# Performance work log

Hardware: AMD Instinct MI355X
Metric: run time of the kernel (lower is better)

## Reference

```python
import jax, jax.numpy as jnp
import numpy as np

N = 50000      # nodes
E = 800000     # edges
F = 128        # num_features
H = 128        # hidden_channels
L = 3          # num_layers
P = 32         # num_partitions
EPS = 1e-5     # BatchNorm1d eps


def _batchnorm(h):
    # BatchNorm1d(affine=False, track_running_stats=False): batch stats, biased var
    m = jnp.mean(h, axis=0)
    v = jnp.var(h, axis=0)
    return (h - m) * jax.lax.rsqrt(v + EPS)


def setup_inputs() -> dict:
    key = jax.random.key(0)
    ks = jax.random.split(key, 12)
    x = jax.random.normal(ks[0], (N, F), dtype=jnp.float32)
    edge_index = jax.random.randint(ks[1], (2, E), 0, N)
    edge_weights = jax.random.uniform(ks[2], (E,), dtype=jnp.float32)
    partitions = (jax.random.uniform(ks[3], (N, P)) < (1.0 / P)).astype(jnp.float32)
    node_weights = jax.random.uniform(ks[4], (N,), dtype=jnp.float32)
    edge_curr_node = jax.random.uniform(ks[5], (N,), dtype=jnp.float32)
    conv_w = 0.05 * jax.random.normal(ks[6], (L, F, H), dtype=jnp.float32)
    conv_b = jnp.zeros((L, H), dtype=jnp.float32)
    lin1_w = 0.05 * jax.random.normal(ks[7], (4 * H, H), dtype=jnp.float32)
    lin1_b = jnp.zeros((H,), dtype=jnp.float32)
    lin2_w = 0.05 * jax.random.normal(ks[8], (H, 1), dtype=jnp.float32)
    lin2_b = jnp.zeros((1,), dtype=jnp.float32)
    return {"x": x, "edge_index": edge_index, "edge_weights": edge_weights,
            "partitions": partitions, "node_weights": node_weights,
            "edge_curr_node": edge_curr_node, "conv_w": conv_w, "conv_b": conv_b,
            "lin1_w": lin1_w, "lin1_b": lin1_b, "lin2_w": lin2_w,
            "lin2_b": lin2_b, "curr_node_id": 123}


def reference(x, edge_index, edge_weights, partitions, node_weights,
              edge_curr_node, conv_w, conv_b, lin1_w, lin1_b, lin2_w, lin2_b,
              curr_node_id):
    src, dst = edge_index[0], edge_index[1]
    # GCN normalization with added self-loops (weight 1)
    deg = jax.ops.segment_sum(edge_weights, dst, num_segments=N) + 1.0
    dinv = jax.lax.rsqrt(deg)
    norm = dinv[src] * edge_weights * dinv[dst]          # [E]
    self_norm = (dinv * dinv)[:, None]                   # [N,1]

    h = x
    for l in range(L):
        hw = h @ conv_w[l] + conv_b[l]                   # [N,H]
        agg = jax.ops.segment_sum(hw[src] * norm[:, None], dst, num_segments=N)
        agg = agg + hw * self_norm                       # self-loop term
        h = jax.nn.relu(_batchnorm(agg))

    x_curr = h[curr_node_id]                             # [H]
    # mlp scoring: concat [h | x_curr | edge_col repeated to 2H] -> [N,4H]
    cat = jnp.concatenate([
        h,
        jnp.broadcast_to(x_curr[None, :], (N, H)),
        jnp.broadcast_to(edge_curr_node[:, None], (N, 2 * H)),
    ], axis=1)
    scores = jax.nn.relu(cat @ lin1_w + lin1_b) @ lin2_w + lin2_b  # [N,1]
    # pool == 'sum'
    partition_scores = scores.T @ partitions             # [1,P]
    return (partition_scores, h)
```

## Files before the change

### kernel.cpp

```cpp
#include <hip/hip_runtime.h>

#define N_NODES 50000
#define N_EDGES 800000
#define NP 50048
#define MAXDEG 64
#define PADK 136
#define NCOPY 64
#define WPB 512
#define NBUK 196
#define BCAP 6144
#define EBB 782

typedef __bf16 bf16_8 __attribute__((ext_vector_type(8)));
typedef float  f32_4  __attribute__((ext_vector_type(4)));

__device__ inline float2 bf2f2(unsigned int u) {
    union { unsigned int i; float f; } a, b;
    a.i = u << 16;
    b.i = u & 0xffff0000u;
    return make_float2(a.f, b.f);
}

__global__ void k_init_wprep(float* __restrict__ colpart, float* __restrict__ out_head,
                             const float* __restrict__ conv_w, const float* __restrict__ lin1_w,
                             __bf16* __restrict__ WT, float* __restrict__ svec,
                             int* __restrict__ bcnt) {
    int b = blockIdx.x, t = threadIdx.x;
    if (b < WPB) {
        int mat = b >> 7, n = b & 127;
        if (t < 128) {
            const float* srcm = (mat < 3) ? (conv_w + (size_t)mat * 16384) : lin1_w;
            WT[((size_t)mat * 128 + n) * 128 + t] = (__bf16)srcm[(size_t)t * 128 + n];
        }
    } else if (b == WPB) {
        if (t < 128) {
            float s = 0.f;
            for (int k = 256; k < 512; ++k) s += lin1_w[(size_t)k * 128 + t];
            svec[t] = s;
        }
    } else if (b < WPB + 65) {
        int i = (b - WPB - 1) * 256 + t;
        colpart[i] = 0.f;
    } else {
        if (t < 32) out_head[t] = 0.f;
        for (int i = t; i < NBUK * 16; i += 256) bcnt[i] = 0;
    }
}

__global__ __launch_bounds__(1024) void k_bucket(const int* __restrict__ src,
                                                 const int* __restrict__ dst,
                                                 const float* __restrict__ ew,
                                                 int* __restrict__ bcnt,
                                                 uint2* __restrict__ ebuf) {
    __shared__ uint2 stage[1024];
    __shared__ int cnt[NBUK], cnt2[NBUK], lstart[NBUK], gb[NBUK];
    __shared__ int wtot[4];
    int t = threadIdx.x;
    int e0 = blockIdx.x * 1024;
    int tot = min(1024, N_EDGES - e0);
    if (t < NBUK) { cnt[t] = 0; cnt2[t] = 0; }
    __syncthreads();
    uint2 rec = make_uint2(0u, 0u); int b = -1;
    if (t < tot) {
        int e = e0 + t;
        unsigned s = (unsigned)src[e], d = (unsigned)dst[e];
        rec = make_uint2(s | (d << 16), __float_as_uint(ew[e]));
        b = (int)(d >> 8);
        atomicAdd(&cnt[b], 1);
    }
    __syncthreads();
    int c = (t < NBUK) ? cnt[t] : 0;
    int x = c;
#pragma unroll
    for (int d2 = 1; d2 < 64; d2 <<= 1) {
        int v = __shfl_up(x, d2, 64);
        if ((t & 63) >= d2) x += v;
    }
    if ((t & 63) == 63 && t < 256) wtot[t >> 6] = x;
    if (t < NBUK && c > 0) gb[t] = atomicAdd(&bcnt[t * 16], c);
    __syncthreads();
    if (t < NBUK) {
        int pre = x - c;
        for (int w = 0; w < (t >> 6); ++w) pre += wtot[w];
        lstart[t] = pre;
    }
    __syncthreads();
    if (t < tot) {
        int r = atomicAdd(&cnt2[b], 1);
        stage[lstart[b] + r] = rec;
    }
    __syncthreads();
    if (t < tot) {
        uint2 v = stage[t];
        int bb = (int)(v.x >> 24);
        int idx = gb[bb] + (t - lstart[bb]);
        if (idx < BCAP) ebuf[(size_t)bb * BCAP + idx] = v;
    }
}

__global__ __launch_bounds__(256) void k_build(const int* __restrict__ bcnt,
                                               const uint2* __restrict__ ebuf,
                                               uint2* __restrict__ esn,
                                               int* __restrict__ fillp,
                                               float* __restrict__ dinv) {
    __shared__ int cnt[256];
    __shared__ float wsum[256];
    int t = threadIdx.x, b = blockIdx.x;
    cnt[t] = 0; wsum[t] = 0.f;
    __syncthreads();
    int m = min(bcnt[b * 16], BCAP);
    for (int i = t; i < m; i += 256) {
        uint2 rec = ebuf[(size_t)b * BCAP + i];
        int d = (int)(rec.x >> 16);
        int local = d & 255;
        int pos = atomicAdd(&cnt[local], 1);
        if (pos < MAXDEG)
            esn[(size_t)d * MAXDEG + pos] = make_uint2(rec.x & 0xffffu, rec.y);
        atomicAdd(&wsum[local], __uint_as_float(rec.y));
    }
    __syncthreads();
    int gn = b * 256 + t;
    if (gn < N_NODES) {
        fillp[gn] = cnt[t];
        dinv[gn] = rsqrtf(1.0f + wsum[t]);
    }
}

template <int AMODE>
__global__ __launch_bounds__(256) void k_gemm_mfma(const float* __restrict__ A,
                                                   const float* __restrict__ mean,
                                                   const float* __restrict__ rstd,
                                                   const __bf16* __restrict__ WT,
                                                   const float* __restrict__ bias,
                                                   __bf16* __restrict__ C, int nrows,
                                                   uint2* __restrict__ esn,
                                                   const int* __restrict__ fillp,
                                                   const float* __restrict__ dinv,
                                                   int gemmBlocks) {
    __shared__ __bf16 As[64 * PADK];
    __shared__ __bf16 Ws[128 * PADK];
    int t = threadIdx.x;
    if (AMODE == 0 && blockIdx.x >= gemmBlocks) {
        int n = ((blockIdx.x - gemmBlocks) * 256 + t) >> 6;
        int lane = t & 63;
        if (n >= N_NODES) return;
        int num = min(fillp[n], MAXDEG);
        if (lane < num) {
            uint2 e = esn[(size_t)n * MAXDEG + lane];
            float w = dinv[(int)e.x] * __uint_as_float(e.y) * dinv[n];
            esn[(size_t)n * MAXDEG + lane] = make_uint2(e.x, __float_as_uint(w));
        }
        return;
    }
    int rowBase = blockIdx.x * 64;
    const uint4* WTg = (const uint4*)WT;
    for (int i = t; i < 2048; i += 256) {
        int n = i >> 4, k8 = i & 15;
        *(uint4*)&Ws[n * PADK + k8 * 8] = WTg[i];
    }
    const float4* A4 = (const float4*)A;
    const float4* M4 = (const float4*)mean;
    const float4* R4 = (const float4*)rstd;
    for (int i = t; i < 1024; i += 256) {
        int r = i >> 4, k8 = i & 15;
        int gr = rowBase + r;
        float4 a0 = make_float4(0.f, 0.f, 0.f, 0.f), a1 = a0;
        if (gr < nrows) {
            a0 = A4[(size_t)gr * 32 + k8 * 2];
            a1 = A4[(size_t)gr * 32 + k8 * 2 + 1];
        }
        if (AMODE == 1) {
            float4 m0 = M4[k8 * 2], m1 = M4[k8 * 2 + 1];
            float4 r0 = R4[k8 * 2], r1 = R4[k8 * 2 + 1];
            a0.x = fmaxf((a0.x - m0.x) * r0.x, 0.f); a0.y = fmaxf((a0.y - m0.y) * r0.y, 0.f);
            a0.z = fmaxf((a0.z - m0.z) * r0.z, 0.f); a0.w = fmaxf((a0.w - m0.w) * r0.w, 0.f);
            a1.x = fmaxf((a1.x - m1.x) * r1.x, 0.f); a1.y = fmaxf((a1.y - m1.y) * r1.y, 0.f);
            a1.z = fmaxf((a1.z - m1.z) * r1.z, 0.f); a1.w = fmaxf((a1.w - m1.w) * r1.w, 0.f);
        }
        bf16_8 o = { (__bf16)a0.x, (__bf16)a0.y, (__bf16)a0.z, (__bf16)a0.w,
                     (__bf16)a1.x, (__bf16)a1.y, (__bf16)a1.z, (__bf16)a1.w };
        *(bf16_8*)&As[r * PADK + k8 * 8] = o;
    }
    __syncthreads();
    int wave = t >> 6, lane = t & 63, quad = lane >> 4, m = lane & 15;
    int ar = wave * 16 + m;
    f32_4 acc[8];
#pragma unroll
    for (int i = 0; i < 8; ++i) acc[i] = (f32_4){0.f, 0.f, 0.f, 0.f};
#pragma unroll
    for (int kk = 0; kk < 4; ++kk) {
        bf16_8 a = *(const bf16_8*)&As[ar * PADK + kk * 32 + quad * 8];
#pragma unroll
        for (int n0 = 0; n0 < 8; ++n0) {
            bf16_8 b = *(const bf16_8*)&Ws[(n0 * 16 + m) * PADK + kk * 32 + quad * 8];
            acc[n0] = __builtin_amdgcn_mfma_f32_16x16x32_bf16(a, b, acc[n0], 0, 0, 0);
        }
    }
    __syncthreads();
#pragma unroll
    for (int n0 = 0; n0 < 8; ++n0) {
        int col = n0 * 16 + m;
        float bi = bias[col];
#pragma unroll
        for (int r = 0; r < 4; ++r) {
            int rr = wave * 16 + quad * 4 + r;
            As[rr * PADK + col] = (__bf16)(acc[n0][r] + bi);
        }
    }
    __syncthreads();
    uint4* Cg = (uint4*)C;
    for (int i = t; i < 1024; i += 256) {
        int r = i >> 4, k8 = i & 15;
        int gr = rowBase + r;
        if (gr < nrows) Cg[(size_t)gr * 16 + k8] = *(const uint4*)&As[r * PADK + k8 * 8];
    }
}

__global__ __launch_bounds__(256) void k_agg(const __bf16* __restrict__ hwb,
                                             const uint2* __restrict__ esn,
                                             const int* __restrict__ fillp,
                                             const float* __restrict__ dinv,
                                             float* __restrict__ agg,
                                             float* __restrict__ colpart) {
    __shared__ float red1[4 * 128], red2[4 * 128];
    int t = threadIdx.x;
    int n = (blockIdx.x * 256 + t) >> 6;
    int lane = t & 63, wave = t >> 6;
    int rs = lane >> 4, c16 = lane & 15;
    float acc[8];
#pragma unroll
    for (int k = 0; k < 8; ++k) acc[k] = 0.f;
    const uint4* hwq = (const uint4*)hwb;
    if (n < N_NODES) {
        int num = min(fillp[n], MAXDEG);
        float dvn = dinv[n];
        uint4 sv = hwq[(size_t)n * 16 + c16];
        int s_l = 0; float w_l = 0.f;
        if (lane < num) {
            uint2 e = esn[(size_t)n * MAXDEG + lane];
            s_l = (int)e.x;
            w_l = __uint_as_float(e.y);
        }
        int groups = (num + 3) >> 2;
        int g = 0;
        for (; g + 4 <= groups; g += 4) {
            uint4 u[4]; float w[4];
#pragma unroll
            for (int j = 0; j < 4; ++j) {
                int idx = (g + j) * 4 + rs;
                int s = __shfl(s_l, idx, 64);
                w[j] = __shfl(w_l, idx, 64);
                u[j] = hwq[(size_t)s * 16 + c16];
            }
#pragma unroll
            for (int j = 0; j < 4; ++j) {
                float2 f0 = bf2f2(u[j].x), f1 = bf2f2(u[j].y);
                float2 f2 = bf2f2(u[j].z), f3 = bf2f2(u[j].w);
                acc[0] += f0.x * w[j]; acc[1] += f0.y * w[j];
                acc[2] += f1.x * w[j]; acc[3] += f1.y * w[j];
                acc[4] += f2.x * w[j]; acc[5] += f2.y * w[j];
                acc[6] += f3.x * w[j]; acc[7] += f3.y * w[j];
            }
        }
        for (; g < groups; ++g) {
            int idx = g * 4 + rs;
            int s = __shfl(s_l, idx, 64);
            float w = __shfl(w_l, idx, 64);
            uint4 u = hwq[(size_t)s * 16 + c16];
            float2 f0 = bf2f2(u.x), f1 = bf2f2(u.y), f2 = bf2f2(u.z), f3 = bf2f2(u.w);
            acc[0] += f0.x * w; acc[1] += f0.y * w;
            acc[2] += f1.x * w; acc[3] += f1.y * w;
            acc[4] += f2.x * w; acc[5] += f2.y * w;
            acc[6] += f3.x * w; acc[7] += f3.y * w;
        }
#pragma unroll
        for (int k = 0; k < 8; ++k) {
            acc[k] += __shfl_xor(acc[k], 16, 64);
            acc[k] += __shfl_xor(acc[k], 32, 64);
        }
        float d2 = dvn * dvn;
        float2 s0 = bf2f2(sv.x), s1 = bf2f2(sv.y), s2 = bf2f2(sv.z), s3 = bf2f2(sv.w);
        acc[0] += s0.x * d2; acc[1] += s0.y * d2;
        acc[2] += s1.x * d2; acc[3] += s1.y * d2;
        acc[4] += s2.x * d2; acc[5] += s2.y * d2;
        acc[6] += s3.x * d2; acc[7] += s3.y * d2;
        if (rs < 2) {
            float4 o = make_float4(acc[rs * 4 + 0], acc[rs * 4 + 1],
                                   acc[rs * 4 + 2], acc[rs * 4 + 3]);
            ((float4*)agg)[(size_t)n * 32 + c16 * 2 + rs] = o;
        }
    }
    if (rs == 0) {
        *(float4*)&red1[wave * 128 + c16 * 8 + 0] =
            make_float4(acc[0], acc[1], acc[2], acc[3]);
        *(float4*)&red1[wave * 128 + c16 * 8 + 4] =
            make_float4(acc[4], acc[5], acc[6], acc[7]);
        *(float4*)&red2[wave * 128 + c16 * 8 + 0] =
            make_float4(acc[0] * acc[0], acc[1] * acc[1], acc[2] * acc[2], acc[3] * acc[3]);
        *(float4*)&red2[wave * 128 + c16 * 8 + 4] =
            make_float4(acc[4] * acc[4], acc[5] * acc[5], acc[6] * acc[6], acc[7] * acc[7]);
    }
    __syncthreads();
    if (t < 128) {
        float s = red1[t] + red1[128 + t] + red1[256 + t] + red1[384 + t];
        float q = red2[t] + red2[128 + t] + red2[256 + t] + red2[384 + t];
        int c = blockIdx.x & (NCOPY - 1);
        unsafeAtomicAdd(&colpart[c * 128 + t], s);
        unsafeAtomicAdd(&colpart[NCOPY * 128 + c * 128 + t], q);
    }
}

__global__ void k_bnfinal(float* colpart, float* mean, float* rstd) {
    int j = threadIdx.x;
    float s = 0.f, q = 0.f;
    for (int c = 0; c < NCOPY; ++c) {
        s += colpart[c * 128 + j];
        q += colpart[NCOPY * 128 + c * 128 + j];
        colpart[c * 128 + j] = 0.f;
        colpart[NCOPY * 128 + c * 128 + j] = 0.f;
    }
    float m = s * (1.0f / N_NODES);
    float v = q * (1.0f / N_NODES) - m * m;
    mean[j] = m;
    rstd[j] = rsqrtf(v + 1e-5f);
}

__global__ void k_prep(const float* __restrict__ agg, const float* __restrict__ mean,
                       const float* __restrict__ rstd, const int* __restrict__ cid,
                       const float* __restrict__ lin1w, const float* __restrict__ lin1b,
                       float* c0) {
    __shared__ float xc[128];
    int t = threadIdx.x;
    int cn = cid[0];
    float a = agg[(size_t)cn * 128 + t];
    xc[t] = fmaxf((a - mean[t]) * rstd[t], 0.f);
    __syncthreads();
    float acc = lin1b[t];
    for (int k = 0; k < 128; ++k)
        acc += xc[k] * lin1w[(size_t)(128 + k) * 128 + t];
    c0[t] = acc;
}

__global__ __launch_bounds__(256) void k_score_mfma(const float* __restrict__ agg,
                                                    const float* __restrict__ mean,
                                                    const float* __restrict__ rstd,
                                                    const __bf16* __restrict__ WT,
                                                    const float* __restrict__ c0,
                                                    const float* __restrict__ svec,
                                                    const float* __restrict__ ecn,
                                                    const float* __restrict__ lin2w,
                                                    const float* __restrict__ lin2b,
                                                    float* __restrict__ scores,
                                                    float* __restrict__ hout,
                                                    int nrows) {
    __shared__ __bf16 As[64 * PADK];
    __shared__ __bf16 Ws[128 * PADK];
    __shared__ float c0s[128], svs[128], l2s[128];
    int t = threadIdx.x;
    int rowBase = blockIdx.x * 64;
    const uint4* WTg = (const uint4*)WT;
    for (int i = t; i < 2048; i += 256) {
        int n = i >> 4, k8 = i & 15;
        *(uint4*)&Ws[n * PADK + k8 * 8] = WTg[i];
    }
    const float4* A4 = (const float4*)agg;
    const float4* M4 = (const float4*)mean;
    const float4* R4 = (const float4*)rstd;
    float4* H4 = (float4*)hout;
    for (int i = t; i < 1024; i += 256) {
        int r = i >> 4, k8 = i & 15;
        int gr = rowBase + r;
        float4 a0 = make_float4(0.f, 0.f, 0.f, 0.f), a1 = a0;
        if (gr < nrows) {
            a0 = A4[(size_t)gr * 32 + k8 * 2];
            a1 = A4[(size_t)gr * 32 + k8 * 2 + 1];
        }
        float4 m0 = M4[k8 * 2], m1 = M4[k8 * 2 + 1];
        float4 r0 = R4[k8 * 2], r1 = R4[k8 * 2 + 1];
        float4 f0, f1;
        f0.x = fmaxf((a0.x - m0.x) * r0.x, 0.f); f0.y = fmaxf((a0.y - m0.y) * r0.y, 0.f);
        f0.z = fmaxf((a0.z - m0.z) * r0.z, 0.f); f0.w = fmaxf((a0.w - m0.w) * r0.w, 0.f);
        f1.x = fmaxf((a1.x - m1.x) * r1.x, 0.f); f1.y = fmaxf((a1.y - m1.y) * r1.y, 0.f);
        f1.z = fmaxf((a1.z - m1.z) * r1.z, 0.f); f1.w = fmaxf((a1.w - m1.w) * r1.w, 0.f);
        if (gr < nrows) {
            H4[(size_t)gr * 32 + k8 * 2] = f0;
            H4[(size_t)gr * 32 + k8 * 2 + 1] = f1;
        }
        bf16_8 o = { (__bf16)f0.x, (__bf16)f0.y, (__bf16)f0.z, (__bf16)f0.w,
                     (__bf16)f1.x, (__bf16)f1.y, (__bf16)f1.z, (__bf16)f1.w };
        *(bf16_8*)&As[r * PADK + k8 * 8] = o;
    }
    if (t < 128) { c0s[t] = c0[t]; svs[t] = svec[t]; l2s[t] = lin2w[t]; }
    __syncthreads();
    int wave = t >> 6, lane = t & 63, quad = lane >> 4, m = lane & 15;
    int ar = wave * 16 + m;
    f32_4 acc[8];
#pragma unroll
    for (int i = 0; i < 8; ++i) acc[i] = (f32_4){0.f, 0.f, 0.f, 0.f};
#pragma unroll
    for (int kk = 0; kk < 4; ++kk) {
        bf16_8 a = *(const bf16_8*)&As[ar * PADK + kk * 32 + quad * 8];
#pragma unroll
        for (int n0 = 0; n0 < 8; ++n0) {
            bf16_8 b = *(const bf16_8*)&Ws[(n0 * 16 + m) * PADK + kk * 32 + quad * 8];
            acc[n0] = __builtin_amdgcn_mfma_f32_16x16x32_bf16(a, b, acc[n0], 0, 0, 0);
        }
    }
    float l2b = lin2b[0];
#pragma unroll
    for (int r = 0; r < 4; ++r) {
        int row = rowBase + wave * 16 + quad * 4 + r;
        float e = (row < nrows) ? ecn[row] : 0.f;
        float partial = 0.f;
#pragma unroll
        for (int n0 = 0; n0 < 8; ++n0) {
            int col = n0 * 16 + m;
            float v = acc[n0][r] + c0s[col] + e * svs[col];
            partial += fmaxf(v, 0.f) * l2s[col];
        }
        partial += __shfl_xor(partial, 8, 16);
        partial += __shfl_xor(partial, 4, 16);
        partial += __shfl_xor(partial, 2, 16);
        partial += __shfl_xor(partial, 1, 16);
        if (m == 0 && row < nrows) scores[row] = partial + l2b;
    }
}

__global__ void k_partition(const float* __restrict__ scores, const float* __restrict__ part,
                            float* out) {
    __shared__ float red[256];
    int t = threadIdx.x;
    int p = t & 31, rg = t >> 5;
    float acc = 0.f;
    for (int r = blockIdx.x * 8 + rg; r < N_NODES; r += gridDim.x * 8)
        acc += scores[r] * part[(size_t)r * 32 + p];
    red[t] = acc;
    __syncthreads();
    if (t < 32) {
        float s = 0.f;
        for (int i = 0; i < 8; ++i) s += red[i * 32 + t];
        unsafeAtomicAdd(&out[t], s);
    }
}

extern "C" void kernel_launch(void* const* d_in, const int* in_sizes, int n_in,
                              void* d_out, int out_size, void* d_ws, size_t ws_size,
                              hipStream_t stream) {
    const float* x        = (const float*)d_in[0];
    const int*   eidx     = (const int*)d_in[1];
    const float* ew       = (const float*)d_in[2];
    const float* parts    = (const float*)d_in[3];
    const float* ecn      = (const float*)d_in[5];
    const float* conv_w   = (const float*)d_in[6];
    const float* conv_b   = (const float*)d_in[7];
    const float* lin1_w   = (const float*)d_in[8];
    const float* lin1_b   = (const float*)d_in[9];
    const float* lin2_w   = (const float*)d_in[10];
    const float* lin2_b   = (const float*)d_in[11];
    const int*   cid      = (const int*)d_in[12];

    const int* src = eidx;
    const int* dst = eidx + N_EDGES;

    char* p = (char*)d_ws;
    auto alloc = [&](size_t bytes) { char* r = p; p += (bytes + 255) & ~size_t(255); return r; };
    int*    fillp   = (int*)alloc((size_t)NP * 4);
    uint2*  esn     = (uint2*)alloc((size_t)N_NODES * MAXDEG * 8);
    float*  dinv    = (float*)alloc(NP * 4);
    float*  scores  = (float*)alloc(NP * 4);
    float*  colpart = (float*)alloc(2 * NCOPY * 128 * 4);
    float*  mean    = (float*)alloc(128 * 4);
    float*  rstd    = (float*)alloc(128 * 4);
    float*  c0      = (float*)alloc(128 * 4);
    float*  svec    = (float*)alloc(128 * 4);
    __bf16* WT      = (__bf16*)alloc(4 * 128 * 128 * 2);
    __bf16* hwb     = (__bf16*)alloc((size_t)N_NODES * 128 * 2);
    float*  agg     = (float*)alloc((size_t)N_NODES * 128 * 4);
    int*    bcnt    = (int*)alloc((size_t)NBUK * 16 * 4);
    uint2*  ebuf    = (uint2*)alloc((size_t)NBUK * BCAP * 8);

    float* out_head = (float*)d_out;
    float* hbuf     = (float*)d_out + 32;

    const int GB = (N_NODES + 63) / 64;
    const int AB = (N_NODES * 64 + 255) / 256;

    k_init_wprep<<<WPB + 66, 256, 0, stream>>>(colpart, out_head, conv_w, lin1_w, WT, svec, bcnt);
    k_bucket<<<EBB, 1024, 0, stream>>>(src, dst, ew, bcnt, ebuf);
    k_build<<<NBUK, 256, 0, stream>>>(bcnt, ebuf, esn, fillp, dinv);

    for (int l = 0; l < 3; ++l) {
        if (l == 0)
            k_gemm_mfma<0><<<GB + AB, 256, 0, stream>>>(x, mean, rstd, WT, conv_b, hwb, N_NODES,
                                                        esn, fillp, dinv, GB);
        else
            k_gemm_mfma<1><<<GB, 256, 0, stream>>>(agg, mean, rstd, WT + (size_t)l * 16384,
                                                   conv_b + (size_t)l * 128, hwb, N_NODES,
                                                   nullptr, nullptr, nullptr, GB);
        k_agg<<<AB, 256, 0, stream>>>(hwb, esn, fillp, dinv, agg, colpart);
        k_bnfinal<<<1, 128, 0, stream>>>(colpart, mean, rstd);
    }

    k_prep<<<1, 128, 0, stream>>>(agg, mean, rstd, cid, lin1_w, lin1_b, c0);
    k_score_mfma<<<GB, 256, 0, stream>>>(agg, mean, rstd, WT + (size_t)3 * 16384, c0, svec,
                                         ecn, lin2_w, lin2_b, scores, hbuf, N_NODES);
    k_partition<<<256, 256, 0, stream>>>(scores, parts, out_head);
}
```

Before: 344.3 us.

## Replace padded per-node edge slots with compact CSR-style packed edge list

The per-node adjacency storage moves from a fixed 64-slot padded array to a compact packed array. Row offsets come from a block-local prefix scan over in-degree counts, and k_build makes a second pass over the bucket to scatter edges. Consumers now read edges at rowofs[n]+lane, which shrinks the footprint and should give denser cache lines for edge-list reads. In exchange k_build reads the bucket twice, adds a scan, and performs an extra rowofs load per node.

```diff
diff --git a/kernel.cpp b/kernel.cpp
--- a/kernel.cpp
+++ b/kernel.cpp
@@ -100,28 +100,49 @@
 
 __global__ __launch_bounds__(256) void k_build(const int* __restrict__ bcnt,
                                                const uint2* __restrict__ ebuf,
-                                               uint2* __restrict__ esn,
+                                               uint2* __restrict__ packed,
+                                               int* __restrict__ rowofs,
                                                int* __restrict__ fillp,
                                                float* __restrict__ dinv) {
     __shared__ int cnt[256];
     __shared__ float wsum[256];
+    __shared__ int pos[256];
+    __shared__ int wtot[4];
     int t = threadIdx.x, b = blockIdx.x;
     cnt[t] = 0; wsum[t] = 0.f;
     __syncthreads();
     int m = min(bcnt[b * 16], BCAP);
     for (int i = t; i < m; i += 256) {
         uint2 rec = ebuf[(size_t)b * BCAP + i];
-        int d = (int)(rec.x >> 16);
-        int local = d & 255;
-        int pos = atomicAdd(&cnt[local], 1);
-        if (pos < MAXDEG)
-            esn[(size_t)d * MAXDEG + pos] = make_uint2(rec.x & 0xffffu, rec.y);
+        int local = (int)(rec.x >> 16) & 255;
+        atomicAdd(&cnt[local], 1);
         atomicAdd(&wsum[local], __uint_as_float(rec.y));
     }
     __syncthreads();
+    int c = cnt[t];
+    int x = c;
+#pragma unroll
+    for (int d2 = 1; d2 < 64; d2 <<= 1) {
+        int v = __shfl_up(x, d2, 64);
+        if ((t & 63) >= d2) x += v;
+    }
+    if ((t & 63) == 63) wtot[t >> 6] = x;
+    __syncthreads();
+    int pre = x - c;
+    for (int w = 0; w < (t >> 6); ++w) pre += wtot[w];
+    int rstart = b * BCAP + pre;
+    pos[t] = rstart;
+    __syncthreads();
+    for (int i = t; i < m; i += 256) {
+        uint2 rec = ebuf[(size_t)b * BCAP + i];
+        int local = (int)(rec.x >> 16) & 255;
+        int p = atomicAdd(&pos[local], 1);
+        packed[p] = make_uint2(rec.x & 0xffffu, rec.y);
+    }
     int gn = b * 256 + t;
     if (gn < N_NODES) {
-        fillp[gn] = cnt[t];
+        fillp[gn] = c;
+        rowofs[gn] = rstart;
         dinv[gn] = rsqrtf(1.0f + wsum[t]);
     }
 }
@@ -133,7 +154,8 @@
                                                    const __bf16* __restrict__ WT,
                                                    const float* __restrict__ bias,
                                                    __bf16* __restrict__ C, int nrows,
-                                                   uint2* __restrict__ esn,
+                                                   uint2* __restrict__ packed,
+                                                   const int* __restrict__ rowofs,
                                                    const int* __restrict__ fillp,
                                                    const float* __restrict__ dinv,
                                                    int gemmBlocks) {
@@ -146,9 +168,10 @@
         if (n >= N_NODES) return;
         int num = min(fillp[n], MAXDEG);
         if (lane < num) {
-            uint2 e = esn[(size_t)n * MAXDEG + lane];
+            int ro = rowofs[n];
+            uint2 e = packed[ro + lane];
             float w = dinv[(int)e.x] * __uint_as_float(e.y) * dinv[n];
-            esn[(size_t)n * MAXDEG + lane] = make_uint2(e.x, __float_as_uint(w));
+            packed[ro + lane] = make_uint2(e.x, __float_as_uint(w));
         }
         return;
     }
@@ -217,7 +240,8 @@
 }
 
 __global__ __launch_bounds__(256) void k_agg(const __bf16* __restrict__ hwb,
-                                             const uint2* __restrict__ esn,
+                                             const uint2* __restrict__ packed,
+                                             const int* __restrict__ rowofs,
                                              const int* __restrict__ fillp,
                                              const float* __restrict__ dinv,
                                              float* __restrict__ agg,
@@ -233,11 +257,12 @@
     const uint4* hwq = (const uint4*)hwb;
     if (n < N_NODES) {
         int num = min(fillp[n], MAXDEG);
+        int ro = rowofs[n];
         float dvn = dinv[n];
         uint4 sv = hwq[(size_t)n * 16 + c16];
         int s_l = 0; float w_l = 0.f;
         if (lane < num) {
-            uint2 e = esn[(size_t)n * MAXDEG + lane];
+            uint2 e = packed[ro + lane];
             s_l = (int)e.x;
             w_l = __uint_as_float(e.y);
         }
@@ -465,7 +490,8 @@
     char* p = (char*)d_ws;
     auto alloc = [&](size_t bytes) { char* r = p; p += (bytes + 255) & ~size_t(255); return r; };
     int*    fillp   = (int*)alloc((size_t)NP * 4);
-    uint2*  esn     = (uint2*)alloc((size_t)N_NODES * MAXDEG * 8);
+    int*    rowofs  = (int*)alloc((size_t)NP * 4);
+    uint2*  packed  = (uint2*)alloc((size_t)NBUK * BCAP * 8);
     float*  dinv    = (float*)alloc(NP * 4);
     float*  scores  = (float*)alloc(NP * 4);
     float*  colpart = (float*)alloc(2 * NCOPY * 128 * 4);
@@ -487,17 +513,17 @@
 
     k_init_wprep<<<WPB + 66, 256, 0, stream>>>(colpart, out_head, conv_w, lin1_w, WT, svec, bcnt);
     k_bucket<<<EBB, 1024, 0, stream>>>(src, dst, ew, bcnt, ebuf);
-    k_build<<<NBUK, 256, 0, stream>>>(bcnt, ebuf, esn, fillp, dinv);
+    k_build<<<NBUK, 256, 0, stream>>>(bcnt, ebuf, packed, rowofs, fillp, dinv);
 
     for (int l = 0; l < 3; ++l) {
         if (l == 0)
             k_gemm_mfma<0><<<GB + AB, 256, 0, stream>>>(x, mean, rstd, WT, conv_b, hwb, N_NODES,
-                                                        esn, fillp, dinv, GB);
+                                                        packed, rowofs, fillp, dinv, GB);
         else
             k_gemm_mfma<1><<<GB, 256, 0, stream>>>(agg, mean, rstd, WT + (size_t)l * 16384,
                                                    conv_b + (size_t)l * 128, hwb, N_NODES,
-                                                   nullptr, nullptr, nullptr, GB);
-        k_agg<<<AB, 256, 0, stream>>>(hwb, esn, fillp, dinv, agg, colpart);
+                                                   nullptr, nullptr, nullptr, nullptr, GB);
+        k_agg<<<AB, 256, 0, stream>>>(hwb, packed, rowofs, fillp, dinv, agg, colpart);
         k_bnfinal<<<1, 128, 0, stream>>>(colpart, mean, rstd);
     }
 
```

Result: slower. 354.3 us (+2.9%).
